# Optimization experiments

Hardware: AMD Instinct MI355X
Metric: run time of the kernel (lower is better)

Reference implementation:

```python
import jax, jax.numpy as jnp
import numpy as np

B, N, R, S, FIN, NCLS, KNN = 16, 2048, 64, 64, 6, 40, 40


def _knn_laplacian(x, k):
    # pairwise squared distance -> gaussian affinity -> row-wise top-k sparsify
    # -> symmetric-normalized Laplacian  L = I - D^{-1/2} A D^{-1/2}
    xx = jnp.sum(x * x, axis=-1)                      # [B,N]
    inner = jnp.einsum('bnd,bmd->bnm', x, x)          # [B,N,N]
    dist = xx[:, :, None] + xx[:, None, :] - 2.0 * inner
    A = jnp.exp(-dist)
    kth = jax.lax.top_k(A, k)[0][..., -1]             # k-th largest per row [B,N]
    A = jnp.where(A >= kth[..., None], A, jnp.zeros((), A.dtype))
    d = jnp.sum(A, axis=-1)
    dis = jnp.where(d > 0, jax.lax.rsqrt(jnp.maximum(d, 1e-12)), jnp.zeros((), A.dtype))
    L = jnp.eye(A.shape[-1], dtype=A.dtype) - dis[:, :, None] * A * dis[:, None, :]
    return L


def _cheb_conv(x, L, w, b):
    # DenseChebConv, K=3: T0=x, T1=Lx, T2=2LT1-T0, then linear on concat
    t0 = x
    t1 = jnp.matmul(L, x)
    t2 = 2.0 * jnp.matmul(L, t1) - t0
    xc = jnp.concatenate([t0, t1, t2], axis=-1)       # [B,N,3*Fin]
    return jnp.matmul(xc, w) + b


def setup_inputs() -> dict:
    key = jax.random.key(0)
    ks = jax.random.split(key, 16)
    p = lambda k_, sh: (jax.random.normal(k_, sh, dtype=jnp.float32) * 0.02)
    return {
        'x': jax.random.normal(ks[0], (B, N, FIN), dtype=jnp.float32),
        'laplacian_Reeb': jax.random.normal(ks[1], (B, R, R), dtype=jnp.float32),
        'sccs': jax.random.randint(ks[2], (B, R, S), 0, N),
        'vertices_reeb': jax.random.normal(ks[3], (B * R, 3), dtype=jnp.float32),
        'edges_reeb': jax.random.randint(ks[4], (B, 128, 2), 0, R),
        'labels': jax.random.randint(ks[5], (B,), 0, NCLS),
        'k': KNN, 'batch_size': B, 'num_points': N,
        'conv1_w': p(ks[6], (3 * FIN, 128)), 'conv1_b': jnp.zeros((128,), jnp.float32),
        'conv2_w': p(ks[7], (3 * 128, 512)), 'conv2_b': jnp.zeros((512,), jnp.float32),
        'convReeb_w': p(ks[8], (3 * 128, 512)), 'convReeb_b': jnp.zeros((512,), jnp.float32),
        'fc1_w': p(ks[9], (1024, 512)), 'fc1_b': jnp.zeros((512,), jnp.float32),
        'fc2_w': p(ks[10], (512, 128)), 'fc2_b': jnp.zeros((128,), jnp.float32),
        'fc3_w': p(ks[11], (128, NCLS)), 'fc3_b': jnp.zeros((NCLS,), jnp.float32),
    }


def reference(x, laplacian_Reeb, sccs, vertices_reeb, edges_reeb, labels, k,
              batch_size, num_points, conv1_w, conv1_b, conv2_w, conv2_b,
              convReeb_w, convReeb_b, fc1_w, fc1_b, fc2_w, fc2_b, fc3_w, fc3_b):
    regs = []
    # graph build is under no_grad in the original
    L = jax.lax.stop_gradient(_knn_laplacian(x, k))
    out = jax.nn.relu(_cheb_conv(x, L, conv1_w, conv1_b))           # [B,N,128]
    regs.append(jnp.linalg.norm(jnp.einsum('bnf,bnm,bmg->bfg', out, L, out)) ** 2)

    # Reeb ragged segment-max pool (no_grad in original): gather SCC index
    # groups per Reeb node and max-reduce -> [B,R,128]
    gathered = jax.vmap(lambda o, s: o[s])(out, sccs)               # [B,R,S,128]
    Vertices_final_Reeb = jax.lax.stop_gradient(jnp.max(gathered, axis=2))
    laplacian_Reeb_final = jax.lax.stop_gradient(laplacian_Reeb)

    L2 = jax.lax.stop_gradient(_knn_laplacian(out, k))
    out = jax.nn.relu(_cheb_conv(out, L2, conv2_w, conv2_b))        # [B,N,512]
    regs.append(jnp.linalg.norm(jnp.einsum('bnf,bnm,bmg->bfg', out, L2, out)) ** 2)

    out_Reeb = jax.nn.relu(_cheb_conv(Vertices_final_Reeb, laplacian_Reeb_final,
                                      convReeb_w, convReeb_b))      # [B,R,512]
    regs.append(jnp.linalg.norm(jnp.einsum('brf,brq,bqg->bfg', out_Reeb,
                                           laplacian_Reeb_final, out_Reeb)) ** 2)

    out = jnp.max(out, axis=1)            # [B,512]
    out_Reeb = jnp.max(out_Reeb, axis=1)  # [B,512]
    out = jnp.concatenate([out_Reeb, out], axis=1)                  # [B,1024]

    out = jnp.matmul(out, fc1_w) + fc1_b
    regs.append(jnp.linalg.norm(fc1_w[:, 0]) ** 2); regs.append(fc1_b[0] ** 2)
    out = jax.nn.relu(out)
    out = jnp.matmul(out, fc2_w) + fc2_b
    regs.append(jnp.linalg.norm(fc2_w[:, 0]) ** 2); regs.append(fc2_b[0] ** 2)
    out = jax.nn.relu(out)
    out = jnp.matmul(out, fc3_w) + fc3_b
    regs.append(jnp.linalg.norm(fc3_w[:, 0]) ** 2); regs.append(fc3_b[0] ** 2)
    return out, jnp.stack(regs)
```

## Files before the change

### kernel.cpp

```cpp
#include <hip/hip_runtime.h>

#define NB 16
#define NP 2048
#define NR 64
#define NS 64
#define KSEL 40

typedef __attribute__((ext_vector_type(8))) short bf16x8;
typedef __attribute__((ext_vector_type(4))) float f32x4;

constexpr long aOUT1 = 0;
constexpr long aT1A  = aOUT1 + 16L*2048*128;
constexpr long aT2A  = aT1A  + 16L*2048*6;
constexpr long aZ1   = aT2A  + 16L*2048*6;
constexpr long aVALS1= aZ1   + 16L*2048*128;
constexpr long aDIS1 = aVALS1+ 16L*2048*64;
constexpr long aVALS2= aDIS1 + 16L*2048;
constexpr long aDIS2 = aVALS2+ 16L*2048*64;
constexpr long aXX2  = aDIS2 + 16L*2048;
constexpr long aXX1  = aXX2  + 16L*2048;
constexpr long aG    = aXX1  + 16L*2048;
constexpr long aT1B  = aG    + 16L*2048*2048;
constexpr long aT2B  = aT1B  + 16L*2048*128;
constexpr long aOUT2 = aT2B  + 16L*2048*128;
constexpr long aZ2   = aOUT2 + 16L*2048*512;
constexpr long aVFR  = aZ2   + 16L*2048*512;
constexpr long aT1R  = aVFR  + 16L*64*128;
constexpr long aT2R  = aT1R  + 16L*64*128;
constexpr long aOUTR = aT2R  + 16L*64*128;
constexpr long aZR   = aOUTR + 16L*64*512;
constexpr long aPOOL = aZR   + 16L*64*512;
constexpr long aFC1O = aPOOL + 16L*1024;
constexpr long aFC2O = aFC1O + 16L*512;
constexpr long aMPP  = aFC2O + 16L*128;
constexpr long FTOT  = aMPP  + 16L*8*512;

constexpr long iCOLS1 = 0;
constexpr long iCNT1  = iCOLS1 + 16L*2048*64;
constexpr long iCOLS2 = iCNT1  + 16L*2048;
constexpr long iCNT2  = iCOLS2 + 16L*2048*64;
constexpr long ITOT   = iCNT2  + 16L*2048;

constexpr long uOUT1H = 0;
constexpr long uOUT1L = uOUT1H + 16L*2048*128;
constexpr long uOUT1R = uOUT1L + 16L*2048*128;
constexpr long uT1BH  = uOUT1R + 16L*2048*128;
constexpr long uT1BL  = uT1BH  + 16L*2048*128;
constexpr long uT2BH  = uT1BL  + 16L*2048*128;
constexpr long uT2BL  = uT2BH  + 16L*2048*128;
constexpr long uW2T   = uT2BL  + 16L*2048*128;
constexpr long uVFRH  = uW2T   + 512L*384;
constexpr long uVFRL  = uVFRH  + 16L*64*128;
constexpr long uT1RH  = uVFRL  + 16L*64*128;
constexpr long uT1RL  = uT1RH  + 16L*64*128;
constexpr long uT2RH  = uT1RL  + 16L*64*128;
constexpr long uT2RL  = uT2RH  + 16L*64*128;
constexpr long uWRT   = uT2RL  + 16L*64*128;
constexpr long uOUT1T = uWRT   + 512L*384;
constexpr long uZ1T   = uOUT1T + 16L*128*2048;
constexpr long uOUT2T = uZ1T   + 16L*128*2048;
constexpr long uZ2T   = uOUT2T + 16L*512*2048;
constexpr long uOUTRT = uZ2T   + 16L*512*2048;
constexpr long uZRT   = uOUTRT + 16L*512*64;
constexpr long uOUT2B = uZRT   + 16L*512*64;
constexpr long UTOT   = uOUT2B + 16L*2048*512;

__device__ __align__(256) float  g_farena[FTOT];
__device__ __align__(256) int    g_iarena[ITOT];
__device__ __align__(256) ushort g_uarena[UTOT];

__device__ __forceinline__ float wsum_f(float v){
  #pragma unroll
  for (int s=32;s>0;s>>=1) v += __shfl_xor(v, s, 64);
  return v;
}
__device__ __forceinline__ int wsum_i(int v){
  #pragma unroll
  for (int s=32;s>0;s>>=1) v += __shfl_xor(v, s, 64);
  return v;
}

__device__ __forceinline__ void gl2lds16(const void* g, void* l){
  __builtin_amdgcn_global_load_lds(
      (const __attribute__((address_space(1))) void*)g,
      (__attribute__((address_space(3))) void*)l, 16, 0, 0);
}

__device__ __forceinline__ ushort bf_rne(float x){
  unsigned u = __float_as_uint(x);
  u += 0x7fffu + ((u >> 16) & 1u);
  return (ushort)(u >> 16);
}
__device__ __forceinline__ void bf_hilo(float x, ushort& h, ushort& l){
  unsigned u = __float_as_uint(x);
  h = (ushort)(u >> 16);
  float hf = __uint_as_float(u & 0xffff0000u);
  l = (ushort)(__float_as_uint(x - hf) >> 16);
}

__device__ __forceinline__ void topk_store(float (&dk)[32], int lane, long row,
    int* __restrict__ cols, float* __restrict__ vals,
    int* __restrict__ cnt, float* __restrict__ dis)
{
  float dmin = dk[0], dmax = dk[0];
  #pragma unroll
  for (int q=1;q<32;++q){ dmin = fminf(dmin, dk[q]); dmax = fmaxf(dmax, dk[q]); }
  #pragma unroll
  for (int s=32;s>0;s>>=1){
    dmin = fminf(dmin, __shfl_xor(dmin, s, 64));
    dmax = fmaxf(dmax, __shfl_xor(dmax, s, 64));
  }
  int c0 = 0;
  #pragma unroll
  for (int q=0;q<32;++q) c0 += (int)__popcll(__ballot(dk[q] <= dmin));
  float kth;
  if (c0 >= KSEL){
    kth = dmin;
  } else {
    float lo = dmin, hi = dmax;
    int cLo = c0, cHi = 2048, it = 0;
    while (cHi != KSEL && __float_as_uint(hi) - __float_as_uint(lo) > 1u){
      float t;
      if (it & 1){
        t = __uint_as_float((__float_as_uint(lo) + __float_as_uint(hi)) >> 1);
      } else {
        t = lo + (hi - lo) * ((float)(KSEL - cLo) / (float)(cHi - cLo));
        unsigned tb = __float_as_uint(t);
        unsigned lb = __float_as_uint(lo), hb = __float_as_uint(hi);
        if (tb <= lb) tb = lb + 1u;
        else if (tb >= hb) tb = hb - 1u;
        t = __uint_as_float(tb);
      }
      ++it;
      int c = 0;
      #pragma unroll
      for (int q=0;q<32;++q) c += (int)__popcll(__ballot(dk[q] <= t));
      if (c >= KSEL){ hi = t; cHi = c; } else { lo = t; cLo = c; }
    }
    kth = hi;
  }
  int kc = 0;
  #pragma unroll
  for (int q=0;q<32;++q) kc += (dk[q] <= kth) ? 1 : 0;
  int tot = wsum_i(kc);
  int incl = kc;
  #pragma unroll
  for (int s=1;s<64;s<<=1){ int u = __shfl_up(incl, s, 64); if (lane >= s) incl += u; }
  int pos = incl - kc;
  int* cp = cols + row*64; float* vp = vals + row*64;
  float d = 0.f;
  #pragma unroll
  for (int q=0;q<32;++q){
    if (dk[q] <= kth){
      float v = __expf(-dk[q]);
      d += v;
      if (pos < 64){ cp[pos] = q*64 + lane; vp[pos] = v; }
      pos++;
    }
  }
  d = wsum_f(d);
  if (lane == 0){
    cnt[row] = tot <= 64 ? tot : 64;
    dis[row] = d > 0.f ? (1.0f / sqrtf(fmaxf(d, 1e-12f))) : 0.f;
  }
}

__global__ __launch_bounds__(256) void xx6_kernel(const float* __restrict__ x,
    float* __restrict__ xx1)
{
  long i = (long)blockIdx.x*256 + threadIdx.x;
  const float* p = x + i*6;
  float2 v0 = *(const float2*)(p);
  float2 v1 = *(const float2*)(p+2);
  float2 v2 = *(const float2*)(p+4);
  xx1[i] = v0.x*v0.x + v0.y*v0.y + v1.x*v1.x + v1.y*v1.y + v2.x*v2.x + v2.y*v2.y;
}

__global__ __launch_bounds__(256) void knn1_kernel(const float* __restrict__ x,
    const float* __restrict__ xx1,
    int* __restrict__ cols, float* __restrict__ vals, int* __restrict__ cnt,
    float* __restrict__ dis)
{
  int lane = threadIdx.x & 63;
  long row = (long)blockIdx.x*4 + (threadIdx.x >> 6);
  int b = (int)(row >> 11); int i = (int)(row & (NP-1));
  const float* xb = x + (long)b*NP*6;
  const float* xxb = xx1 + ((long)b << 11);
  float xi[6];
  #pragma unroll
  for (int d2=0; d2<6; ++d2) xi[d2] = xb[(long)i*6 + d2];
  float xxi = xxb[i];
  float dk[32];
  #pragma unroll 4
  for (int c=0;c<32;++c){
    int j = c*64 + lane;
    const float* xj = xb + (long)j*6;
    float2 v0 = *(const float2*)(xj);
    float2 v1 = *(const float2*)(xj+2);
    float2 v2 = *(const float2*)(xj+4);
    float inr = xi[0]*v0.x + xi[1]*v0.y + xi[2]*v1.x + xi[3]*v1.y + xi[4]*v2.x + xi[5]*v2.y;
    dk[c] = fmaxf(xxi + xxb[j] - 2.f*inr, 0.f);
  }
  topk_store(dk, lane, row, cols, vals, cnt, dis);
}

__global__ __launch_bounds__(256) void knn2_kernel(const float* __restrict__ G,
    const float* __restrict__ xx,
    int* __restrict__ cols, float* __restrict__ vals, int* __restrict__ cnt,
    float* __restrict__ dis)
{
  int lane = threadIdx.x & 63;
  long row = (long)blockIdx.x*4 + (threadIdx.x >> 6);
  const float* Gr = G + row*NP;
  const float* xxb = xx + ((row >> 11) << 11);
  int i = (int)(row & (NP-1));
  float xxi = xxb[i];
  float dk[32];
  #pragma unroll 4
  for (int c=0;c<32;++c){
    int j = c*64 + lane;
    dk[c] = fmaxf(xxi + xxb[j] - 2.f*Gr[j], 0.f);
  }
  topk_store(dk, lane, row, cols, vals, cnt, dis);
}

__global__ __launch_bounds__(256) void spmm6_kernel(const float* __restrict__ X,
    const float* __restrict__ T0, float* __restrict__ Y,
    const int* __restrict__ cols, const float* __restrict__ vals,
    const int* __restrict__ cnt, const float* __restrict__ dis,
    float c1, float c2, float cs)
{
  long row = (long)blockIdx.x*256 + threadIdx.x;
  int b = (int)(row >> 11);
  const float* Xb = X + ((long)b << 11)*6;
  const float* db = dis + ((long)b << 11);
  float acc[6] = {0,0,0,0,0,0};
  int c = cnt[row];
  const int* cp = cols + row*64; const float* vp = vals + row*64;
  for (int t=0;t<c;++t){
    int j = cp[t];
    float w = vp[t] * db[j];
    const float* xr = Xb + (long)j*6;
    #pragma unroll
    for (int d2=0; d2<6; ++d2) acc[d2] += w * xr[d2];
  }
  float di = dis[row];
  #pragma unroll
  for (int d2=0; d2<6; ++d2)
    Y[row*6+d2] = c1*X[row*6+d2] + c2*T0[row*6+d2] - cs*di*acc[d2];
}

template<int W, bool PACK>
__global__ __launch_bounds__((W >= 256) ? 256 : W) void spmm_kernel(
    const float* __restrict__ X, const float* __restrict__ T0, float* __restrict__ Y,
    ushort* __restrict__ Hh, ushort* __restrict__ Ll,
    const int* __restrict__ cols, const float* __restrict__ vals,
    const int* __restrict__ cnt, const float* __restrict__ dis,
    float c1, float c2, float cs)
{
  constexpr int TPB = (W >= 256) ? 256 : W;
  constexpr int E = W / TPB;
  __shared__ int scol[64];
  __shared__ float sval[64];
  int q = blockIdx.x;
  long row = ((long)(q & 7) << 12) + (q >> 3);
  int b = (int)(row >> 11);
  int tid = threadIdx.x;
  int c = cnt[row];
  if (tid < 64){ scol[tid] = cols[row*64+tid]; sval[tid] = vals[row*64+tid]; }
  __syncthreads();
  const float* Xb = X + ((long)b << 11)*W;
  const float* db = dis + ((long)b << 11);
  float acc[E] = {};
  for (int t=0;t<c;++t){
    int j = scol[t];
    float w = sval[t] * db[j];
    const float* xr = Xb + (long)j*W;
    #pragma unroll
    for (int e=0;e<E;++e) acc[e] += w * xr[tid + e*TPB];
  }
  float di = dis[row];
  #pragma unroll
  for (int e=0;e<E;++e){
    long idx = row*W + tid + e*TPB;
    float y = c1*X[idx] + c2*T0[idx] - cs*di*acc[e];
    Y[idx] = y;
    if (PACK){
      ushort h, l; bf_hilo(y, h, l);
      Hh[idx] = h; Ll[idx] = l;
    }
  }
}

__global__ __launch_bounds__(256) void spmmb_kernel(
    const float* __restrict__ X, const ushort* __restrict__ Xb,
    float* __restrict__ Y,
    const int* __restrict__ cols, const float* __restrict__ vals,
    const int* __restrict__ cnt, const float* __restrict__ dis)
{
  __shared__ int scol[4][64];
  __shared__ float sval[4][64];
  int q = blockIdx.x;
  int wid = threadIdx.x >> 6, lane = threadIdx.x & 63;
  long row = ((long)(q & 7) << 12) + ((long)(q >> 3) << 2) + wid;
  int b = (int)(row >> 11);
  scol[wid][lane] = cols[row*64 + lane];
  sval[wid][lane] = vals[row*64 + lane];
  const ushort* Xbb = Xb + ((long)b << 11)*512;
  const float* db = dis + ((long)b << 11);
  int c = cnt[row];
  float acc[8] = {};
  for (int t=0;t<c;++t){
    int j = scol[wid][t];
    float w = sval[wid][t] * db[j];
    bf16x8 v = *(const bf16x8*)(Xbb + (long)j*512 + lane*8);
    #pragma unroll
    for (int e=0;e<8;++e)
      acc[e] += w * __uint_as_float(((unsigned)(ushort)v[e]) << 16);
  }
  float di = dis[row];
  long base = row*512 + lane*8;
  float4 x0 = *(const float4*)(X + base);
  float4 x1 = *(const float4*)(X + base + 4);
  float4 o0, o1;
  o0.x = x0.x - di*acc[0]; o0.y = x0.y - di*acc[1];
  o0.z = x0.z - di*acc[2]; o0.w = x0.w - di*acc[3];
  o1.x = x1.x - di*acc[4]; o1.y = x1.y - di*acc[5];
  o1.z = x1.z - di*acc[6]; o1.w = x1.w - di*acc[7];
  *(float4*)(Y + base) = o0;
  *(float4*)(Y + base + 4) = o1;
}

__global__ __launch_bounds__(128) void conv1_kernel(const float* __restrict__ x,
    const float* __restrict__ t1, const float* __restrict__ t2,
    const float* __restrict__ w, const float* __restrict__ bias,
    float* __restrict__ out, ushort* __restrict__ oh, ushort* __restrict__ ol,
    ushort* __restrict__ orr)
{
  long row = blockIdx.x; int o = threadIdx.x;
  float acc = bias[o];
  const float* xr = x + row*6; const float* a1 = t1 + row*6; const float* a2 = t2 + row*6;
  #pragma unroll
  for (int d2=0; d2<6; ++d2){
    acc += xr[d2]*w[d2*128 + o];
    acc += a1[d2]*w[(6+d2)*128 + o];
    acc += a2[d2]*w[(12+d2)*128 + o];
  }
  acc = fmaxf(acc, 0.f);
  long idx = row*128 + o;
  out[idx] = acc;
  ushort h, l; bf_hilo(acc, h, l);
  oh[idx] = h; ol[idx] = l;
  orr[idx] = bf_rne(acc);
}

template<bool HILO>
__global__ __launch_bounds__(256) void tpack_kernel(const float* __restrict__ X,
    ushort* __restrict__ H, ushort* __restrict__ L,
    int R, int C, long sIn, long sOut)
{
  __shared__ float tile[32][33];
  int c0 = blockIdx.x*32, r0 = blockIdx.y*32, b = blockIdx.z;
  const float* Xb = X + (long)b*sIn;
  int tx = threadIdx.x & 31, ty = threadIdx.x >> 5;
  #pragma unroll
  for (int rr=ty; rr<32; rr+=8)
    tile[rr][tx] = Xb[(long)(r0+rr)*C + c0+tx];
  __syncthreads();
  #pragma unroll
  for (int cc=ty; cc<32; cc+=8){
    float xv = tile[tx][cc];
    long oidx = (long)b*sOut + (long)(c0+cc)*R + r0 + tx;
    if (HILO){
      ushort h, l; bf_hilo(xv, h, l);
      H[oidx] = h; L[oidx] = l;
    } else {
      H[oidx] = bf_rne(xv);
    }
  }
}

template<bool SPLITA, bool CHEB, bool BR>
__global__ __launch_bounds__(256) void mgemm_kernel(
    const ushort* __restrict__ Ah0, const ushort* __restrict__ Ah1, const ushort* __restrict__ Ah2,
    const ushort* __restrict__ Al0, const ushort* __restrict__ Al1, const ushort* __restrict__ Al2,
    const ushort* __restrict__ Bh,
    const float* __restrict__ bias, float* __restrict__ C,
    ushort* __restrict__ Cb, float* __restrict__ ssq,
    int M, int N, int K, long sA, long sB, long sC)
{
  __shared__ ushort AsH[128*32];
  __shared__ ushort BsH[128*32];
  __shared__ ushort AsL[SPLITA ? 128*32 : 8];
  int bz = blockIdx.z;
  int m0 = blockIdx.x*128, n0 = blockIdx.y*128;
  int tid = threadIdx.x, lane = tid & 63, wid = tid >> 6;
  int wm = (wid & 1)*64, wn = (wid >> 1)*64;
  f32x4 acc[4][4] = {};
  const ushort* Bb = Bh + (long)bz*sB;
  const ushort* Ab = CHEB ? Ah0 : (Ah0 + (long)bz*sA);
  const ushort* Alb = (SPLITA && !CHEB) ? (Al0 + (long)bz*sA) : Al0;

  for (int k0 = 0; k0 < K; k0 += 32){
    #pragma unroll
    for (int cc2=0; cc2<2; ++cc2){
      int chunk = wid*2 + cc2;
      int e = chunk*512 + lane*8;
      int row = e >> 5;
      int slot = (e >> 3) & 3;
      int scol = (slot ^ ((row >> 1) & 3)) * 8;
      const ushort* asrc;
      if (CHEB){
        int kg2 = k0 + scol;
        const ushort* base = (kg2 < 128) ? Ah0 : ((kg2 < 256) ? Ah1 : Ah2);
        asrc = base + (long)(m0+row)*128 + (kg2 & 127);
      } else {
        asrc = Ab + (long)(m0+row)*K + k0 + scol;
      }
      gl2lds16(asrc, &AsH[chunk*512]);
      gl2lds16(Bb + (long)(n0+row)*K + k0 + scol, &BsH[chunk*512]);
      if (SPLITA){
        const ushort* alsrc;
        if (CHEB){
          int kg2 = k0 + scol;
          const ushort* base = (kg2 < 128) ? Al0 : ((kg2 < 256) ? Al1 : Al2);
          alsrc = base + (long)(m0+row)*128 + (kg2 & 127);
        } else {
          alsrc = Alb + (long)(m0+row)*K + k0 + scol;
        }
        gl2lds16(alsrc, &AsL[chunk*512]);
      }
    }
    __syncthreads();
    int lr = lane & 15, kg = lane >> 4;
    bf16x8 af[4], bfr[4];
    #pragma unroll
    for (int f=0; f<4; ++f){
      int ra = wm + f*16 + lr;
      int rb = wn + f*16 + lr;
      af[f]  = *(const bf16x8*)&AsH[ra*32 + (kg ^ ((ra>>1)&3))*8];
      bfr[f] = *(const bf16x8*)&BsH[rb*32 + (kg ^ ((rb>>1)&3))*8];
    }
    if (SPLITA){
      bf16x8 al[4];
      #pragma unroll
      for (int f=0; f<4; ++f){
        int ra = wm + f*16 + lr;
        al[f] = *(const bf16x8*)&AsL[ra*32 + (kg ^ ((ra>>1)&3))*8];
      }
      #pragma unroll
      for (int mf=0; mf<4; ++mf)
        #pragma unroll
        for (int nf=0; nf<4; ++nf){
          acc[mf][nf] = __builtin_amdgcn_mfma_f32_16x16x32_bf16(af[mf], bfr[nf], acc[mf][nf], 0,0,0);
          acc[mf][nf] = __builtin_amdgcn_mfma_f32_16x16x32_bf16(al[mf], bfr[nf], acc[mf][nf], 0,0,0);
        }
    } else {
      #pragma unroll
      for (int mf=0; mf<4; ++mf)
        #pragma unroll
        for (int nf=0; nf<4; ++nf)
          acc[mf][nf] = __builtin_amdgcn_mfma_f32_16x16x32_bf16(af[mf], bfr[nf], acc[mf][nf], 0,0,0);
    }
    __syncthreads();
  }
  int lr = lane & 15, l4 = (lane >> 4)*4;
  if (ssq){
    float s = 0.f;
    #pragma unroll
    for (int mf=0; mf<4; ++mf)
      #pragma unroll
      for (int nf=0; nf<4; ++nf)
        #pragma unroll
        for (int r=0; r<4; ++r){ float v = acc[mf][nf][r]; s += v*v; }
    s = wsum_f(s);
    if (lane == 0) atomicAdd(ssq, s);
    return;
  }
  #pragma unroll
  for (int mf=0; mf<4; ++mf){
    #pragma unroll
    for (int nf=0; nf<4; ++nf){
      int n = n0 + wn + nf*16 + lr;
      float bv = BR ? bias[n] : 0.f;
      #pragma unroll
      for (int r=0; r<4; ++r){
        int m = m0 + wm + mf*16 + l4 + r;
        float v = acc[mf][nf][r];
        if (BR) v = fmaxf(v + bv, 0.f);
        C[(long)bz*sC + (long)m*N + n] = v;
        if (Cb) Cb[(long)bz*sC + (long)m*N + n] = bf_rne(v);
      }
    }
  }
}

__global__ __launch_bounds__(256) void rownorm_kernel(const float* __restrict__ X,
    float* __restrict__ xx)
{
  int lane = threadIdx.x & 63;
  long row = (long)blockIdx.x*4 + (threadIdx.x >> 6);
  const float* p = X + row*128;
  float v0 = p[lane], v1 = p[64+lane];
  float s = wsum_f(v0*v0 + v1*v1);
  if (lane == 0) xx[row] = s;
}

__global__ __launch_bounds__(128) void reeb_pool_kernel(const float* __restrict__ out1,
    const int* __restrict__ sccs, float* __restrict__ VfR,
    ushort* __restrict__ Hh, ushort* __restrict__ Ll)
{
  int q = blockIdx.x;
  int br = ((q & 7) << 7) + (q >> 3);
  int b = br >> 6;
  int f = threadIdx.x;
  const int* sp = sccs + (long)br*NS;
  const float* ob = out1 + ((long)b << 11)*128;
  float m = -1e30f;
  for (int s=0;s<NS;++s){
    int idx = sp[s];
    m = fmaxf(m, ob[(long)idx*128 + f]);
  }
  long oidx = (long)br*128 + f;
  VfR[oidx] = m;
  ushort h, l; bf_hilo(m, h, l);
  Hh[oidx] = h; Ll[oidx] = l;
}

template<int W, bool PACK>
__global__ __launch_bounds__((W>=256)?256:W) void reeb_mm_kernel(const float* __restrict__ Lap,
    const float* __restrict__ X, const float* __restrict__ T0, float* __restrict__ Y,
    ushort* __restrict__ Hh, ushort* __restrict__ Ll,
    float cs, float c2)
{
  constexpr int TPB = (W>=256)?256:W;
  constexpr int E = W/TPB;
  int br = blockIdx.x; int b = br >> 6; int r = br & 63;
  const float* lr = Lap + ((long)b*NR + r)*NR;
  const float* Xb = X + (long)b*NR*W;
  int tid = threadIdx.x;
  float acc[E] = {};
  for (int q=0;q<NR;++q){
    float w = lr[q];
    #pragma unroll
    for (int e=0;e<E;++e) acc[e] += w * Xb[(long)q*W + tid + e*TPB];
  }
  #pragma unroll
  for (int e=0;e<E;++e){
    long idx = (long)br*W + tid + e*TPB;
    float y = cs*acc[e] + c2*T0[idx];
    Y[idx] = y;
    if (PACK){
      ushort h, l; bf_hilo(y, h, l);
      Hh[idx] = h; Ll[idx] = l;
    }
  }
}

__global__ __launch_bounds__(512) void maxpool1_kernel(const float* __restrict__ X,
    float* __restrict__ part)
{
  int b = blockIdx.x, rc = blockIdx.y; int f = threadIdx.x;
  const float* p = X + ((long)b*2048 + (long)rc*256)*512 + f;
  float m = -1e30f;
  #pragma unroll 4
  for (int r=0;r<256;++r) m = fmaxf(m, p[(long)r*512]);
  part[((long)b*8+rc)*512 + f] = m;
}

__global__ __launch_bounds__(512) void maxpool2_kernel(const float* __restrict__ part,
    const float* __restrict__ outR, float* __restrict__ pool)
{
  int b = blockIdx.x; int f = threadIdx.x;
  const float* pp = part + (long)b*8*512 + f;
  float m = -1e30f;
  #pragma unroll
  for (int r=0;r<8;++r) m = fmaxf(m, pp[r*512]);
  pool[(long)b*1024 + 512 + f] = m;
  const float* rp = outR + (long)b*64*512 + f;
  float mr = -1e30f;
  #pragma unroll 4
  for (int r=0;r<64;++r) mr = fmaxf(mr, rp[(long)r*512]);
  pool[(long)b*1024 + f] = mr;
}

template<bool RELU>
__global__ __launch_bounds__(256) void fc_kernel(const float* __restrict__ in,
    const float* __restrict__ W, const float* __restrict__ bias,
    float* __restrict__ out, int IN, int OUT)
{
  __shared__ float red[4][64];
  int b = blockIdx.x, o0 = blockIdx.y*64;
  int tid = threadIdx.x;
  int ol = tid & 63, q = tid >> 6;
  int o = o0 + ol;
  const float* ip = in + (long)b*IN;
  float acc = 0.f;
  if (o < OUT){
    int kb = IN >> 2;
    int ks = q*kb;
    for (int i=0;i<kb;i+=8){
      #pragma unroll
      for (int u=0;u<8;++u){
        int k = ks + i + u;
        acc += ip[k]*W[(long)k*OUT + o];
      }
    }
  }
  red[q][ol] = acc;
  __syncthreads();
  if (tid < 64){
    int oo = o0 + tid;
    if (oo < OUT){
      float s = red[0][tid]+red[1][tid]+red[2][tid]+red[3][tid] + bias[oo];
      out[(long)b*OUT + oo] = RELU ? fmaxf(s, 0.f) : s;
    }
  }
}

__global__ __launch_bounds__(256) void wreg_kernel(const float* __restrict__ w1,
    const float* __restrict__ b1, const float* __restrict__ w2, const float* __restrict__ b2,
    const float* __restrict__ w3, const float* __restrict__ b3, float* __restrict__ out9)
{
  __shared__ float ps[3][4];
  int tid = threadIdx.x, lane = tid & 63, wid = tid >> 6;
  float s1 = 0.f, s2 = 0.f, s3 = 0.f;
  for (int i=tid;i<1024;i+=256){ float v = w1[(long)i*512]; s1 += v*v; }
  for (int i=tid;i<512;i+=256){ float v = w2[(long)i*128]; s2 += v*v; }
  if (tid < 128){ float v = w3[(long)tid*40]; s3 = v*v; }
  s1 = wsum_f(s1); s2 = wsum_f(s2); s3 = wsum_f(s3);
  if (lane == 0){ ps[0][wid]=s1; ps[1][wid]=s2; ps[2][wid]=s3; }
  __syncthreads();
  if (tid == 0){
    out9[3] = ps[0][0]+ps[0][1]+ps[0][2]+ps[0][3];
    out9[4] = b1[0]*b1[0];
    out9[5] = ps[1][0]+ps[1][1]+ps[1][2]+ps[1][3];
    out9[6] = b2[0]*b2[0];
    out9[7] = ps[2][0]+ps[2][1]+ps[2][2]+ps[2][3];
    out9[8] = b3[0]*b3[0];
  }
}

extern "C" void kernel_launch(void* const* d_in, const int* in_sizes, int n_in,
                              void* d_out, int out_size, void* d_ws, size_t ws_size,
                              hipStream_t stream)
{
  (void)in_sizes; (void)n_in; (void)d_ws; (void)ws_size; (void)out_size;
  const float* x    = (const float*)d_in[0];
  const float* lapR = (const float*)d_in[1];
  const int*   sccs = (const int*)d_in[2];
  const float* w1   = (const float*)d_in[9];
  const float* b1   = (const float*)d_in[10];
  const float* w2   = (const float*)d_in[11];
  const float* b2   = (const float*)d_in[12];
  const float* wR   = (const float*)d_in[13];
  const float* bRb  = (const float*)d_in[14];
  const float* fw1  = (const float*)d_in[15];
  const float* fb1  = (const float*)d_in[16];
  const float* fw2  = (const float*)d_in[17];
  const float* fb2  = (const float*)d_in[18];
  const float* fw3  = (const float*)d_in[19];
  const float* fb3  = (const float*)d_in[20];
  float* out = (float*)d_out;

  float* Fb = nullptr; int* Ib = nullptr; ushort* Ub = nullptr;
  hipGetSymbolAddress((void**)&Fb, HIP_SYMBOL(g_farena));
  hipGetSymbolAddress((void**)&Ib, HIP_SYMBOL(g_iarena));
  hipGetSymbolAddress((void**)&Ub, HIP_SYMBOL(g_uarena));

  float* out1 = Fb + aOUT1;  float* t1a = Fb + aT1A;  float* t2a = Fb + aT2A;
  float* Z1   = Fb + aZ1;
  float* vals1= Fb + aVALS1; float* dis1= Fb + aDIS1;
  float* vals2= Fb + aVALS2; float* dis2= Fb + aDIS2;
  float* xx2  = Fb + aXX2;   float* xx1 = Fb + aXX1;  float* G  = Fb + aG;
  float* t1b  = Fb + aT1B;   float* t2b = Fb + aT2B;
  float* out2 = Fb + aOUT2;  float* Z2  = Fb + aZ2;
  float* VfR  = Fb + aVFR;   float* t1R = Fb + aT1R;  float* t2R= Fb + aT2R;
  float* outR = Fb + aOUTR;  float* ZR  = Fb + aZR;
  float* pool = Fb + aPOOL;  float* fc1o= Fb + aFC1O; float* fc2o=Fb + aFC2O;
  float* mpp  = Fb + aMPP;
  int* cols1 = Ib + iCOLS1; int* cnt1 = Ib + iCNT1;
  int* cols2 = Ib + iCOLS2; int* cnt2 = Ib + iCNT2;
  ushort* out1h = Ub + uOUT1H; ushort* out1l = Ub + uOUT1L;
  ushort* out1r = Ub + uOUT1R;
  ushort* t1bh  = Ub + uT1BH;  ushort* t1bl  = Ub + uT1BL;
  ushort* t2bh  = Ub + uT2BH;  ushort* t2bl  = Ub + uT2BL;
  ushort* w2t   = Ub + uW2T;
  ushort* vfrh  = Ub + uVFRH;  ushort* vfrl  = Ub + uVFRL;
  ushort* t1rh  = Ub + uT1RH;  ushort* t1rl  = Ub + uT1RL;
  ushort* t2rh  = Ub + uT2RH;  ushort* t2rl  = Ub + uT2RL;
  ushort* wrt   = Ub + uWRT;
  ushort* out1t = Ub + uOUT1T; ushort* z1t   = Ub + uZ1T;
  ushort* out2t = Ub + uOUT2T; ushort* z2t   = Ub + uZ2T;
  ushort* outrt = Ub + uOUTRT; ushort* zrt   = Ub + uZRT;
  ushort* out2b = Ub + uOUT2B;

  hipMemsetAsync(out + 640, 0, 9*sizeof(float), stream);

  xx6_kernel<<<dim3(128),dim3(256),0,stream>>>(x, xx1);
  knn1_kernel<<<dim3(8192),dim3(256),0,stream>>>(x, xx1, cols1, vals1, cnt1, dis1);
  spmm6_kernel<<<dim3(128),dim3(256),0,stream>>>(x, x, t1a, cols1, vals1, cnt1, dis1, 1.f, 0.f, 1.f);
  spmm6_kernel<<<dim3(128),dim3(256),0,stream>>>(t1a, x, t2a, cols1, vals1, cnt1, dis1, 2.f, -1.f, 2.f);
  conv1_kernel<<<dim3(32768),dim3(128),0,stream>>>(x, t1a, t2a, w1, b1, out1, out1h, out1l, out1r);

  spmm_kernel<128,false><<<dim3(32768),dim3(128),0,stream>>>(out1, out1, Z1, nullptr, nullptr,
      cols1, vals1, cnt1, dis1, 1.f, 0.f, 1.f);
  tpack_kernel<false><<<dim3(4,64,16),dim3(256),0,stream>>>(out1, out1t, nullptr, 2048,128, 2048L*128, 128L*2048);
  tpack_kernel<false><<<dim3(4,64,16),dim3(256),0,stream>>>(Z1,   z1t,   nullptr, 2048,128, 2048L*128, 128L*2048);
  mgemm_kernel<false,false,false><<<dim3(1,1,16),dim3(256),0,stream>>>(
      out1t,nullptr,nullptr, nullptr,nullptr,nullptr, z1t, nullptr, nullptr,
      nullptr, out+640, 128,128,2048, 128L*2048, 128L*2048, 0);
  reeb_pool_kernel<<<dim3(1024),dim3(128),0,stream>>>(out1, sccs, VfR, vfrh, vfrl);

  rownorm_kernel<<<dim3(8192),dim3(256),0,stream>>>(out1, xx2);
  mgemm_kernel<false,false,false><<<dim3(16,16,16),dim3(256),0,stream>>>(
      out1r,nullptr,nullptr, nullptr,nullptr,nullptr, out1r, nullptr, G,
      nullptr, nullptr, 2048,2048,128, (long)NP*128, (long)NP*128, (long)NP*NP);
  knn2_kernel<<<dim3(8192),dim3(256),0,stream>>>(G, xx2, cols2, vals2, cnt2, dis2);

  spmm_kernel<128,true><<<dim3(32768),dim3(128),0,stream>>>(out1, out1, t1b, t1bh, t1bl,
      cols2, vals2, cnt2, dis2, 1.f, 0.f, 1.f);
  spmm_kernel<128,true><<<dim3(32768),dim3(128),0,stream>>>(t1b, out1, t2b, t2bh, t2bl,
      cols2, vals2, cnt2, dis2, 2.f, -1.f, 2.f);
  tpack_kernel<false><<<dim3(16,12,1),dim3(256),0,stream>>>(w2, w2t, nullptr, 384,512, 0,0);
  mgemm_kernel<true,true,true><<<dim3(256,4,1),dim3(256),0,stream>>>(
      out1h,t1bh,t2bh, out1l,t1bl,t2bl, w2t, b2, out2,
      out2b, nullptr, 32768,512,384, 0,0,0);
  spmmb_kernel<<<dim3(8192),dim3(256),0,stream>>>(out2, out2b, Z2, cols2, vals2, cnt2, dis2);
  tpack_kernel<false><<<dim3(16,64,16),dim3(256),0,stream>>>(out2, out2t, nullptr, 2048,512, 2048L*512, 512L*2048);
  tpack_kernel<false><<<dim3(16,64,16),dim3(256),0,stream>>>(Z2,   z2t,   nullptr, 2048,512, 2048L*512, 512L*2048);
  mgemm_kernel<false,false,false><<<dim3(4,4,16),dim3(256),0,stream>>>(
      out2t,nullptr,nullptr, nullptr,nullptr,nullptr, z2t, nullptr, nullptr,
      nullptr, out+641, 512,512,2048, 512L*2048, 512L*2048, 0);

  reeb_mm_kernel<128,true><<<dim3(1024),dim3(128),0,stream>>>(lapR, VfR, VfR, t1R, t1rh, t1rl, 1.f, 0.f);
  reeb_mm_kernel<128,true><<<dim3(1024),dim3(128),0,stream>>>(lapR, t1R, VfR, t2R, t2rh, t2rl, 2.f, -1.f);
  tpack_kernel<false><<<dim3(16,12,1),dim3(256),0,stream>>>(wR, wrt, nullptr, 384,512, 0,0);
  mgemm_kernel<true,true,true><<<dim3(8,4,1),dim3(256),0,stream>>>(
      vfrh,t1rh,t2rh, vfrl,t1rl,t2rl, wrt, bRb, outR,
      nullptr, nullptr, 1024,512,384, 0,0,0);
  reeb_mm_kernel<512,false><<<dim3(1024),dim3(256),0,stream>>>(lapR, outR, outR, ZR, nullptr, nullptr, 1.f, 0.f);
  tpack_kernel<false><<<dim3(16,2,16),dim3(256),0,stream>>>(outR, outrt, nullptr, 64,512, 64L*512, 512L*64);
  tpack_kernel<false><<<dim3(16,2,16),dim3(256),0,stream>>>(ZR,   zrt,   nullptr, 64,512, 64L*512, 512L*64);
  mgemm_kernel<false,false,false><<<dim3(4,4,16),dim3(256),0,stream>>>(
      outrt,nullptr,nullptr, nullptr,nullptr,nullptr, zrt, nullptr, nullptr,
      nullptr, out+642, 512,512,64, 512L*64, 512L*64, 0);

  maxpool1_kernel<<<dim3(16,8),dim3(512),0,stream>>>(out2, mpp);
  maxpool2_kernel<<<dim3(16),dim3(512),0,stream>>>(mpp, outR, pool);
  fc_kernel<true ><<<dim3(16,8),dim3(256),0,stream>>>(pool, fw1, fb1, fc1o, 1024, 512);
  fc_kernel<true ><<<dim3(16,2),dim3(256),0,stream>>>(fc1o, fw2, fb2, fc2o, 512, 128);
  fc_kernel<false><<<dim3(16,1),dim3(256),0,stream>>>(fc2o, fw3, fb3, out, 128, 40);
  wreg_kernel<<<dim3(1),dim3(256),0,stream>>>(fw1, fb1, fw2, fb2, fw3, fb3, out+640);
}
```

Baseline: 1.098 ms.

## Split-K the regularizer GEMMs and store Gram matrix as bf16

The two bfnm regularizer GEMMs (128x128x2048 and 512x512x2048 per batch) now use split-K across extra grid blocks. Each split writes a partial result to a scratch buffer, and a new reduction kernel sums the partials, squares them and atomically adds the result. This is meant to fix the low occupancy of the 16-block and 256-block launches. Separately, the 2048x2048 Gram matrix used for kNN2 is now written as bf16 instead of fp32, halving its write and read traffic. The cost is extra scratch memory and a reduction pass, plus a risk of changed top-k neighbor selection from bf16 rounding of distances.

```diff
diff --git a/kernel.cpp b/kernel.cpp
--- a/kernel.cpp
+++ b/kernel.cpp
@@ -19,8 +19,7 @@
 constexpr long aDIS2 = aVALS2+ 16L*2048*64;
 constexpr long aXX2  = aDIS2 + 16L*2048;
 constexpr long aXX1  = aXX2  + 16L*2048;
-constexpr long aG    = aXX1  + 16L*2048;
-constexpr long aT1B  = aG    + 16L*2048*2048;
+constexpr long aT1B  = aXX1  + 16L*2048;
 constexpr long aT2B  = aT1B  + 16L*2048*128;
 constexpr long aOUT2 = aT2B  + 16L*2048*128;
 constexpr long aZ2   = aOUT2 + 16L*2048*512;
@@ -33,7 +32,9 @@
 constexpr long aFC1O = aPOOL + 16L*1024;
 constexpr long aFC2O = aFC1O + 16L*512;
 constexpr long aMPP  = aFC2O + 16L*128;
-constexpr long FTOT  = aMPP  + 16L*8*512;
+constexpr long aM1P  = aMPP  + 16L*8*512;
+constexpr long aM2P  = aM1P  + 8L*16*128*128;
+constexpr long FTOT  = aM2P  + 4L*16*512*512;
 
 constexpr long iCOLS1 = 0;
 constexpr long iCNT1  = iCOLS1 + 16L*2048*64;
@@ -63,7 +64,8 @@
 constexpr long uOUTRT = uZ2T   + 16L*512*2048;
 constexpr long uZRT   = uOUTRT + 16L*512*64;
 constexpr long uOUT2B = uZRT   + 16L*512*64;
-constexpr long UTOT   = uOUT2B + 16L*2048*512;
+constexpr long uG     = uOUT2B + 16L*2048*512;
+constexpr long UTOT   = uG     + 16L*2048*2048;
 
 __device__ __align__(256) float  g_farena[FTOT];
 __device__ __align__(256) int    g_iarena[ITOT];
@@ -96,6 +98,9 @@
   h = (ushort)(u >> 16);
   float hf = __uint_as_float(u & 0xffff0000u);
   l = (ushort)(__float_as_uint(x - hf) >> 16);
+}
+__device__ __forceinline__ float bf2f(ushort u){
+  return __uint_as_float(((unsigned)u) << 16);
 }
 
 __device__ __forceinline__ void topk_store(float (&dk)[32], int lane, long row,
@@ -204,14 +209,14 @@
   topk_store(dk, lane, row, cols, vals, cnt, dis);
 }
 
-__global__ __launch_bounds__(256) void knn2_kernel(const float* __restrict__ G,
+__global__ __launch_bounds__(256) void knn2_kernel(const ushort* __restrict__ G,
     const float* __restrict__ xx,
     int* __restrict__ cols, float* __restrict__ vals, int* __restrict__ cnt,
     float* __restrict__ dis)
 {
   int lane = threadIdx.x & 63;
   long row = (long)blockIdx.x*4 + (threadIdx.x >> 6);
-  const float* Gr = G + row*NP;
+  const ushort* Gr = G + row*NP;
   const float* xxb = xx + ((row >> 11) << 11);
   int i = (int)(row & (NP-1));
   float xxi = xxb[i];
@@ -219,7 +224,7 @@
   #pragma unroll 4
   for (int c=0;c<32;++c){
     int j = c*64 + lane;
-    dk[c] = fmaxf(xxi + xxb[j] - 2.f*Gr[j], 0.f);
+    dk[c] = fmaxf(xxi + xxb[j] - 2.f*bf2f(Gr[j]), 0.f);
   }
   topk_store(dk, lane, row, cols, vals, cnt, dis);
 }
@@ -316,7 +321,7 @@
     bf16x8 v = *(const bf16x8*)(Xbb + (long)j*512 + lane*8);
     #pragma unroll
     for (int e=0;e<8;++e)
-      acc[e] += w * __uint_as_float(((unsigned)(ushort)v[e]) << 16);
+      acc[e] += w * bf2f((ushort)v[e]);
   }
   float di = dis[row];
   long base = row*512 + lane*8;
@@ -387,12 +392,21 @@
     const ushort* __restrict__ Bh,
     const float* __restrict__ bias, float* __restrict__ C,
     ushort* __restrict__ Cb, float* __restrict__ ssq,
-    int M, int N, int K, long sA, long sB, long sC)
+    int M, int N, int K, long sA, long sB, long sC,
+    int kchunk, long sSplit)
 {
   __shared__ ushort AsH[128*32];
   __shared__ ushort BsH[128*32];
   __shared__ ushort AsL[SPLITA ? 128*32 : 8];
   int bz = blockIdx.z;
+  int kb = 0, ke = K;
+  long coff = 0;
+  if (kchunk > 0){
+    int split = bz >> 4; bz &= 15;
+    kb = split * kchunk;
+    ke = kb + kchunk; if (ke > K) ke = K;
+    coff = (long)split * sSplit;
+  }
   int m0 = blockIdx.x*128, n0 = blockIdx.y*128;
   int tid = threadIdx.x, lane = tid & 63, wid = tid >> 6;
   int wm = (wid & 1)*64, wn = (wid >> 1)*64;
@@ -401,7 +415,7 @@
   const ushort* Ab = CHEB ? Ah0 : (Ah0 + (long)bz*sA);
   const ushort* Alb = (SPLITA && !CHEB) ? (Al0 + (long)bz*sA) : Al0;
 
-  for (int k0 = 0; k0 < K; k0 += 32){
+  for (int k0 = kb; k0 < ke; k0 += 32){
     #pragma unroll
     for (int cc2=0; cc2<2; ++cc2){
       int chunk = wid*2 + cc2;
@@ -488,11 +502,29 @@
         int m = m0 + wm + mf*16 + l4 + r;
         float v = acc[mf][nf][r];
         if (BR) v = fmaxf(v + bv, 0.f);
-        C[(long)bz*sC + (long)m*N + n] = v;
+        if (C)  C[coff + (long)bz*sC + (long)m*N + n] = v;
         if (Cb) Cb[(long)bz*sC + (long)m*N + n] = bf_rne(v);
       }
     }
   }
+}
+
+__global__ __launch_bounds__(256) void redssq_kernel(const float* __restrict__ P,
+    long n, int S, long stride, float* __restrict__ tgt)
+{
+  __shared__ float ps[4];
+  long i = (long)blockIdx.x*256 + threadIdx.x;
+  float s = 0.f;
+  if (i < n){
+    float v = 0.f;
+    for (int q=0;q<S;++q) v += P[i + (long)q*stride];
+    s = v*v;
+  }
+  s = wsum_f(s);
+  int lane = threadIdx.x & 63, wid = threadIdx.x >> 6;
+  if (lane == 0) ps[wid] = s;
+  __syncthreads();
+  if (threadIdx.x == 0) atomicAdd(tgt, ps[0]+ps[1]+ps[2]+ps[3]);
 }
 
 __global__ __launch_bounds__(256) void rownorm_kernel(const float* __restrict__ X,
@@ -672,13 +704,13 @@
   float* Z1   = Fb + aZ1;
   float* vals1= Fb + aVALS1; float* dis1= Fb + aDIS1;
   float* vals2= Fb + aVALS2; float* dis2= Fb + aDIS2;
-  float* xx2  = Fb + aXX2;   float* xx1 = Fb + aXX1;  float* G  = Fb + aG;
+  float* xx2  = Fb + aXX2;   float* xx1 = Fb + aXX1;
   float* t1b  = Fb + aT1B;   float* t2b = Fb + aT2B;
   float* out2 = Fb + aOUT2;  float* Z2  = Fb + aZ2;
   float* VfR  = Fb + aVFR;   float* t1R = Fb + aT1R;  float* t2R= Fb + aT2R;
   float* outR = Fb + aOUTR;  float* ZR  = Fb + aZR;
   float* pool = Fb + aPOOL;  float* fc1o= Fb + aFC1O; float* fc2o=Fb + aFC2O;
-  float* mpp  = Fb + aMPP;
+  float* mpp  = Fb + aMPP;   float* M1p = Fb + aM1P;  float* M2p = Fb + aM2P;
   int* cols1 = Ib + iCOLS1; int* cnt1 = Ib + iCNT1;
   int* cols2 = Ib + iCOLS2; int* cnt2 = Ib + iCNT2;
   ushort* out1h = Ub + uOUT1H; ushort* out1l = Ub + uOUT1L;
@@ -693,7 +725,7 @@
   ushort* out1t = Ub + uOUT1T; ushort* z1t   = Ub + uZ1T;
   ushort* out2t = Ub + uOUT2T; ushort* z2t   = Ub + uZ2T;
   ushort* outrt = Ub + uOUTRT; ushort* zrt   = Ub + uZRT;
-  ushort* out2b = Ub + uOUT2B;
+  ushort* out2b = Ub + uOUT2B; ushort* Gb16  = Ub + uG;
 
   hipMemsetAsync(out + 640, 0, 9*sizeof(float), stream);
 
@@ -707,16 +739,17 @@
       cols1, vals1, cnt1, dis1, 1.f, 0.f, 1.f);
   tpack_kernel<false><<<dim3(4,64,16),dim3(256),0,stream>>>(out1, out1t, nullptr, 2048,128, 2048L*128, 128L*2048);
   tpack_kernel<false><<<dim3(4,64,16),dim3(256),0,stream>>>(Z1,   z1t,   nullptr, 2048,128, 2048L*128, 128L*2048);
-  mgemm_kernel<false,false,false><<<dim3(1,1,16),dim3(256),0,stream>>>(
-      out1t,nullptr,nullptr, nullptr,nullptr,nullptr, z1t, nullptr, nullptr,
-      nullptr, out+640, 128,128,2048, 128L*2048, 128L*2048, 0);
+  mgemm_kernel<false,false,false><<<dim3(1,1,128),dim3(256),0,stream>>>(
+      out1t,nullptr,nullptr, nullptr,nullptr,nullptr, z1t, nullptr, M1p,
+      nullptr, nullptr, 128,128,2048, 128L*2048, 128L*2048, 128L*128, 256, 16L*128*128);
+  redssq_kernel<<<dim3(1024),dim3(256),0,stream>>>(M1p, 16L*128*128, 8, 16L*128*128, out+640);
   reeb_pool_kernel<<<dim3(1024),dim3(128),0,stream>>>(out1, sccs, VfR, vfrh, vfrl);
 
   rownorm_kernel<<<dim3(8192),dim3(256),0,stream>>>(out1, xx2);
   mgemm_kernel<false,false,false><<<dim3(16,16,16),dim3(256),0,stream>>>(
-      out1r,nullptr,nullptr, nullptr,nullptr,nullptr, out1r, nullptr, G,
-      nullptr, nullptr, 2048,2048,128, (long)NP*128, (long)NP*128, (long)NP*NP);
-  knn2_kernel<<<dim3(8192),dim3(256),0,stream>>>(G, xx2, cols2, vals2, cnt2, dis2);
+      out1r,nullptr,nullptr, nullptr,nullptr,nullptr, out1r, nullptr, nullptr,
+      Gb16, nullptr, 2048,2048,128, (long)NP*128, (long)NP*128, (long)NP*NP, 0, 0);
+  knn2_kernel<<<dim3(8192),dim3(256),0,stream>>>(Gb16, xx2, cols2, vals2, cnt2, dis2);
 
   spmm_kernel<128,true><<<dim3(32768),dim3(128),0,stream>>>(out1, out1, t1b, t1bh, t1bl,
       cols2, vals2, cnt2, dis2, 1.f, 0.f, 1.f);
@@ -725,26 +758,27 @@
   tpack_kernel<false><<<dim3(16,12,1),dim3(256),0,stream>>>(w2, w2t, nullptr, 384,512, 0,0);
   mgemm_kernel<true,true,true><<<dim3(256,4,1),dim3(256),0,stream>>>(
       out1h,t1bh,t2bh, out1l,t1bl,t2bl, w2t, b2, out2,
-      out2b, nullptr, 32768,512,384, 0,0,0);
+      out2b, nullptr, 32768,512,384, 0,0,0, 0, 0);
   spmmb_kernel<<<dim3(8192),dim3(256),0,stream>>>(out2, out2b, Z2, cols2, vals2, cnt2, dis2);
   tpack_kernel<false><<<dim3(16,64,16),dim3(256),0,stream>>>(out2, out2t, nullptr, 2048,512, 2048L*512, 512L*2048);
   tpack_kernel<false><<<dim3(16,64,16),dim3(256),0,stream>>>(Z2,   z2t,   nullptr, 2048,512, 2048L*512, 512L*2048);
-  mgemm_kernel<false,false,false><<<dim3(4,4,16),dim3(256),0,stream>>>(
-      out2t,nullptr,nullptr, nullptr,nullptr,nullptr, z2t, nullptr, nullptr,
-      nullptr, out+641, 512,512,2048, 512L*2048, 512L*2048, 0);
+  mgemm_kernel<false,false,false><<<dim3(4,4,64),dim3(256),0,stream>>>(
+      out2t,nullptr,nullptr, nullptr,nullptr,nullptr, z2t, nullptr, M2p,
+      nullptr, nullptr, 512,512,2048, 512L*2048, 512L*2048, 512L*512, 512, 16L*512*512);
+  redssq_kernel<<<dim3(16384),dim3(256),0,stream>>>(M2p, 16L*512*512, 4, 16L*512*512, out+641);
 
   reeb_mm_kernel<128,true><<<dim3(1024),dim3(128),0,stream>>>(lapR, VfR, VfR, t1R, t1rh, t1rl, 1.f, 0.f);
   reeb_mm_kernel<128,true><<<dim3(1024),dim3(128),0,stream>>>(lapR, t1R, VfR, t2R, t2rh, t2rl, 2.f, -1.f);
   tpack_kernel<false><<<dim3(16,12,1),dim3(256),0,stream>>>(wR, wrt, nullptr, 384,512, 0,0);
   mgemm_kernel<true,true,true><<<dim3(8,4,1),dim3(256),0,stream>>>(
       vfrh,t1rh,t2rh, vfrl,t1rl,t2rl, wrt, bRb, outR,
-      nullptr, nullptr, 1024,512,384, 0,0,0);
+      nullptr, nullptr, 1024,512,384, 0,0,0, 0, 0);
   reeb_mm_kernel<512,false><<<dim3(1024),dim3(256),0,stream>>>(lapR, outR, outR, ZR, nullptr, nullptr, 1.f, 0.f);
   tpack_kernel<false><<<dim3(16,2,16),dim3(256),0,stream>>>(outR, outrt, nullptr, 64,512, 64L*512, 512L*64);
   tpack_kernel<false><<<dim3(16,2,16),dim3(256),0,stream>>>(ZR,   zrt,   nullptr, 64,512, 64L*512, 512L*64);
   mgemm_kernel<false,false,false><<<dim3(4,4,16),dim3(256),0,stream>>>(
       outrt,nullptr,nullptr, nullptr,nullptr,nullptr, zrt, nullptr, nullptr,
-      nullptr, out+642, 512,512,64, 512L*64, 512L*64, 0);
+      nullptr, out+642, 512,512,64, 512L*64, 512L*64, 0, 0, 0);
 
   maxpool1_kernel<<<dim3(16,8),dim3(512),0,stream>>>(out2, mpp);
   maxpool2_kernel<<<dim3(16),dim3(512),0,stream>>>(mpp, outR, pool);
```

Measured after the change: 1.246 ms. 1.13x slower.
